# Kernel optimization log

Measured on AMD Instinct MI355X. Metric: run time of the kernel, lower is better.

The kernel has to match this reference:

```python
import jax, jax.numpy as jnp
import numpy as np
from jax.scipy.special import erfc

# ---- model constants (mirroring NeuroNN.__init__ defaults) ----
NEURON_NUM = 6000
RATIO = 0.8
NE = int(NEURON_NUM * RATIO)   # excitatory count (pref ordering: E first)
NI = NEURON_NUM - NE           # inhibitory count (connection blocks: first NI rows/cols)
SCALING_G = 1.0
W_FF = 30.0
SIG_EXT = 5.0
TAU = 1.0
TAU_REF = 1.0
T_INV = 1.0
VT, VR = 20.0, 10.0            # LIF threshold / reset (mV) used inside Ricciardi Phi
DT = 0.1
NMAX = 80                      # Euler2fixedpt total steps (fixed for jit)
NAVG = 30                      # convergence-averaging window
XTOL = 1e-5
XMIN = 1.0

# 64-pt Gauss-Legendre quadrature for the Ricciardi integral
_qn, _qw = np.polynomial.legendre.leggauss(64)
QN = jnp.asarray(_qn, jnp.float32)
QW = jnp.asarray(_qw, jnp.float32)
SQRT_PI = float(np.sqrt(np.pi))


def erfcx(y):
    """Scaled complementary error function exp(y^2)*erfc(y), fp32-safe."""
    y = jnp.clip(y, -9.0, 25.0)  # exp(81) still finite in fp32
    a = jnp.abs(y)
    a_s = jnp.minimum(a, 5.0)
    small = jnp.exp(a_s * a_s) * erfc(a_s)
    a_l = jnp.maximum(a, 5.0)
    large = (1.0 / (SQRT_PI * a_l)) * (1.0 - 0.5 / (a_l * a_l))
    f = jnp.where(a <= 5.0, small, large)
    return jnp.where(y >= 0.0, f, 2.0 * jnp.exp(y * y) - f)


def circ_gauss(x_deg, w):
    # circular gaussian with period 180 deg, same form as the z-row kernel
    return jnp.exp((jnp.cos(x_deg * jnp.pi / 90.0) - 1.0) / (4.0 * (jnp.pi / 180.0 * w) ** 2))


def phi(mu, sigma, tau, tau_ref):
    """Ricciardi LIF transfer: 1/(tau_ref + tau*sqrt(pi)*int_l^u erfcx(-x) dx)."""
    u = (VT - mu) / sigma
    l = (VR - mu) / sigma
    c = 0.5 * (u + l)
    h = 0.5 * (u - l)
    x = c[:, None] + h[:, None] * QN[None, :]          # [N, 64]
    integ = h * jnp.sum(QW[None, :] * erfcx(-x), axis=1)
    return 1.0 / (tau_ref + tau * SQRT_PI * jnp.maximum(integ, 0.0))


def setup_inputs() -> dict:
    key = jax.random.key(0)
    k1, k2, k3 = jax.random.split(key, 3)
    # hyperparameters = [J; P; w], exactly the module's init values
    hyperparameters = jnp.array([[1.99, 1.9, -1.01, -0.79],
                                 [0.11, 0.11, 0.45, 0.45],
                                 [32.0, 32.0, 32.0, 32.0]], dtype=jnp.float32)
    contrast = jax.random.uniform(k1, (1,), jnp.float32)                 # [0,1)
    grating_orientations = jax.random.uniform(k2, (1,), jnp.float32) * 180.0
    # self.pref: E then I linspace over [0,180)
    pref = np.concatenate([np.linspace(0.0, 180.0, NE, endpoint=False),
                           np.linspace(0.0, 180.0, NI, endpoint=False)]).astype(np.float32)
    preferred_orientations = jnp.asarray(pref)
    rand_u = jax.random.uniform(k3, (NEURON_NUM, NEURON_NUM), jnp.float32)
    return {"hyperparameters": hyperparameters, "contrast": contrast,
            "grating_orientations": grating_orientations,
            "preferred_orientations": preferred_orientations, "rand_u": rand_u}


def reference(hyperparameters, contrast, grating_orientations, preferred_orientations, rand_u):
    N = NEURON_NUM
    eff_p, prob_p, width_p = hyperparameters[0], hyperparameters[1], hyperparameters[2]
    i = jnp.arange(N)
    ri = (i < NI).astype(jnp.int32)                      # row block (1 if row < NI)
    conn = ri[:, None] + 2 * ri[None, :]                 # 0/1/2/3 block ids [N,N]
    # circulant roll: np.roll(z_row, i)[j] = z_row[(j-i) % N]
    idx = (i[None, :] - i[:, None]) % N                  # [N,N]
    conn_rolled = ri[:, None] + 2 * (idx < NI).astype(jnp.int32)
    thetas = jnp.linspace(0.0, jnp.pi - 0.01, N)
    cos_term = (jnp.cos(2.0 * thetas) - 1.0)[idx]        # gathered, rolled per row
    width_r = width_p[conn_rolled]
    Z = jnp.exp(cos_term / (4.0 * (jnp.pi / 180.0 * width_r) ** 2))
    # W[i,j] = J * sigmoid(32*(P * z_roll - U))
    W = eff_p[conn] * jax.nn.sigmoid(32.0 * (prob_p[conn] * Z - rand_u))
    W2 = W * W
    # stimulus -> feedforward input
    input_mean = contrast * 20.0 * SCALING_G * circ_gauss(
        grating_orientations - preferred_orientations, W_FF)          # [N]
    input_sd = SIG_EXT

    def step(r, _):
        mu = TAU * (W @ r) + input_mean
        sig = jnp.sqrt(TAU * (W2 @ r) + input_sd ** 2)
        dx = T_INV * (phi(mu, sig, TAU, TAU_REF) - r) * DT
        r2 = r + dx
        conv = jnp.max(jnp.abs(dx) / jnp.maximum(XMIN, jnp.abs(r2))) < XTOL
        return r2, conv

    r0 = jnp.zeros(N, jnp.float32)
    r_fp, convs = jax.lax.scan(step, r0, None, length=NMAX)
    avg_step = jnp.mean(convs[-NAVG:].astype(jnp.float32))
    return r_fp, avg_step
```

## Files before the change

### kernel.cpp

```cpp
#include <hip/hip_runtime.h>
#include <hip/hip_fp16.h>
#include <math.h>

#define NN    6000
#define NPAD  6144
#define NIB   1200
#define NMAXI 80
#define NAVGI 30
#define NBLK  250
#define NTHR  768

#define SQRT_PI_F 1.7724538509055160273f

typedef _Float16 half2_t __attribute__((ext_vector_type(2)));
typedef unsigned uvec8  __attribute__((ext_vector_type(8)));

__device__ __forceinline__ float erfcx_ref(float y) {
  y = fminf(fmaxf(y, -9.0f), 25.0f);
  float a   = fabsf(y);
  float a_s = fminf(a, 5.0f);
  float fsm = expf(a_s * a_s) * erfcf(a_s);
  float a_l = fmaxf(a, 5.0f);
  float flg = (1.0f / (SQRT_PI_F * a_l)) * (1.0f - 0.5f / (a_l * a_l));
  float f   = (a <= 5.0f) ? fsm : flg;
  return (y >= 0.0f) ? f : 2.0f * expf(y * y) - f;
}

__device__ __forceinline__ float dot2acc(unsigned w, unsigned r, float acc) {
#if defined(__has_builtin) && __has_builtin(__builtin_amdgcn_fdot2)
  return __builtin_amdgcn_fdot2(__builtin_bit_cast(half2_t, w),
                                __builtin_bit_cast(half2_t, r), acc, false);
#else
  half2_t wh = __builtin_bit_cast(half2_t, w);
  half2_t rh = __builtin_bit_cast(half2_t, r);
  return acc + (float)wh.x * (float)rh.x + (float)wh.y * (float)rh.y;
#endif
}

__device__ __forceinline__ unsigned pksq(unsigned w) {
  half2_t wh = __builtin_bit_cast(half2_t, w);
  half2_t s  = wh * wh;
  return __builtin_bit_cast(unsigned, s);
}

__device__ __forceinline__ void gbar(unsigned* cnt, unsigned* gen, int tid) {
  __syncthreads();
  if (tid == 0) {
    __builtin_amdgcn_fence(__ATOMIC_RELEASE, "agent");
    const unsigned g = __hip_atomic_load(gen, __ATOMIC_RELAXED,
                                         __HIP_MEMORY_SCOPE_AGENT);
    const unsigned old = __hip_atomic_fetch_add(cnt, 1u, __ATOMIC_RELAXED,
                                                __HIP_MEMORY_SCOPE_AGENT);
    if (old == NBLK - 1) {
      __hip_atomic_store(cnt, 0u, __ATOMIC_RELAXED, __HIP_MEMORY_SCOPE_AGENT);
      __hip_atomic_store(gen, g + 1u, __ATOMIC_RELEASE,
                         __HIP_MEMORY_SCOPE_AGENT);
    } else {
      while (__hip_atomic_load(gen, __ATOMIC_RELAXED,
                               __HIP_MEMORY_SCOPE_AGENT) == g)
        __builtin_amdgcn_s_sleep(2);
    }
    __builtin_amdgcn_fence(__ATOMIC_ACQUIRE, "agent");
  }
  __syncthreads();
}

__global__ __launch_bounds__(256) void init_kernel(
    const float* __restrict__ contrast, const float* __restrict__ grat,
    const float* __restrict__ pref, float* __restrict__ g0,
    float* __restrict__ g1, float* __restrict__ meanv,
    float* __restrict__ ctab, float* __restrict__ qn, float* __restrict__ qw,
    unsigned* __restrict__ conv, unsigned* __restrict__ bar)
{
  int t = blockIdx.x * 256 + threadIdx.x;
  if (t < NPAD) { g0[t] = 0.0f; g1[t] = 0.0f; }
  if (t < NN) {
    double th = (3.141592653589793 - 0.01) * (double)t / 5999.0;
    ctab[t] = cosf(2.0f * (float)th) - 1.0f;
    float d  = grat[0] - pref[t];
    float cg = (cosf(d * 3.14159265358979323846f / 90.0f) - 1.0f) / 1.0966227112321508f;
    meanv[t] = contrast[0] * 20.0f * expf(cg);
  }
  if (t < NMAXI) conv[t] = 0u;
  if (t < 2)     bar[t]  = 0u;
  if (blockIdx.x == 0 && threadIdx.x < 64) {
    int m = threadIdx.x;
    double x = cos(3.141592653589793 * (m + 0.75) / 64.5);
    double p0, p1, dp = 1.0;
    for (int it = 0; it < 60; ++it) {
      p0 = 1.0; p1 = x;
      for (int k = 2; k <= 64; ++k) {
        double p2 = ((2.0 * k - 1.0) * x * p1 - (k - 1.0) * p0) / (double)k;
        p0 = p1; p1 = p2;
      }
      dp = 64.0 * (x * p1 - p0) / (x * x - 1.0);
      double step = p1 / dp;
      x -= step;
      if (fabs(step) < 1e-15) break;
    }
    p0 = 1.0; p1 = x;
    for (int k = 2; k <= 64; ++k) {
      double p2 = ((2.0 * k - 1.0) * x * p1 - (k - 1.0) * p0) / (double)k;
      p0 = p1; p1 = p2;
    }
    dp = 64.0 * (x * p1 - p0) / (x * x - 1.0);
    double wgt = 2.0 / ((1.0 - x * x) * dp * dp);
    qn[63 - m] = (float)x;
    qw[63 - m] = (float)wgt;
  }
}

#define GENV(WV, ROW, V, EI, EE, PI, PE, DI, DE, UROW)                        \
  do {                                                                        \
    _Pragma("unroll")                                                         \
    for (int c_ = 0; c_ < 4; ++c_) {                                          \
      const int k_  = (V) * 4 + c_;                                           \
      const int j0_ = k_ * 256 + (lane << 2);                                 \
      float w_[4] = {0.0f, 0.0f, 0.0f, 0.0f};                                 \
      if (j0_ + 3 < NN) {                                                     \
        const float4 uv_ = *reinterpret_cast<const float4*>((UROW) + j0_);    \
        const float us_[4] = {uv_.x, uv_.y, uv_.z, uv_.w};                    \
        _Pragma("unroll")                                                     \
        for (int q_ = 0; q_ < 4; ++q_) {                                      \
          const int j_ = j0_ + q_;                                            \
          int idx_ = j_ - (ROW); idx_ += (idx_ < 0) ? NN : 0;                 \
          const float ct_   = ctabs[idx_];                                    \
          const float eff_  = (j_   < NIB) ? (EI) : (EE);                     \
          const float prob_ = (j_   < NIB) ? (PI) : (PE);                     \
          const float den_  = (idx_ < NIB) ? (DI) : (DE);                     \
          const float Z_  = expf(ct_ / den_);                                 \
          const float tt_ = 32.0f * (prob_ * Z_ - us_[q_]);                   \
          w_[q_] = eff_ / (1.0f + expf(-tt_));                                \
        }                                                                     \
      }                                                                       \
      half2_t h01_; h01_.x = (_Float16)w_[0]; h01_.y = (_Float16)w_[1];       \
      half2_t h23_; h23_.x = (_Float16)w_[2]; h23_.y = (_Float16)w_[3];       \
      WV[2 * c_]     = __builtin_bit_cast(unsigned, h01_);                    \
      WV[2 * c_ + 1] = __builtin_bit_cast(unsigned, h23_);                    \
    }                                                                         \
  } while (0)

#define ACC2(WAV, WBV, V)                                                     \
  do {                                                                        \
    _Pragma("unroll")                                                         \
    for (int c_ = 0; c_ < 4; ++c_) {                                          \
      const uint2 rr_ = rh2[((V) * 4 + c_) * 64 + lane];                      \
      muA  = dot2acc(WAV[2 * c_],       rr_.x, muA);                          \
      muA  = dot2acc(WAV[2 * c_ + 1],   rr_.y, muA);                          \
      varA = dot2acc(pksq(WAV[2 * c_]),     rr_.x, varA);                     \
      varA = dot2acc(pksq(WAV[2 * c_ + 1]), rr_.y, varA);                     \
      muB  = dot2acc(WBV[2 * c_],       rr_.x, muB);                          \
      muB  = dot2acc(WBV[2 * c_ + 1],   rr_.y, muB);                          \
      varB = dot2acc(pksq(WBV[2 * c_]),     rr_.x, varB);                     \
      varB = dot2acc(pksq(WBV[2 * c_ + 1]), rr_.y, varB);                     \
    }                                                                         \
  } while (0)

__global__ __launch_bounds__(NTHR, 3) void solve_kernel(
    const float* __restrict__ hyper, const float* __restrict__ randu,
    const float* __restrict__ ctab, const float* __restrict__ meanv,
    const float* __restrict__ qn, const float* __restrict__ qw,
    float* __restrict__ g0, float* __restrict__ g1,
    float* __restrict__ blkmax, unsigned* __restrict__ bar,
    float* __restrict__ out)
{
  const int tid  = threadIdx.x;
  const int lane = tid & 63;
  const int wv   = tid >> 6;
  const int rowA = blockIdx.x * 24 + wv * 2;
  const int rowB = rowA + 1;

  __shared__ float ctabs[NN];
  __shared__ uint2 rh2[NPAD / 4];
  __shared__ float wmax[12];
  __shared__ float sflag[NAVGI];

  {
    const float4* c4 = reinterpret_cast<const float4*>(ctab);
    float4* l4 = reinterpret_cast<float4*>(ctabs);
    for (int i = tid; i < NN / 4; i += NTHR) l4[i] = c4[i];
  }
  __syncthreads();

  const float qnl = qn[lane];
  const float qwl = qw[lane];
  const float meanA = meanv[rowA];
  const float meanB = meanv[rowB];

  uvec8 wa0, wa1, wa2, wa3, wa4, wa5, wb0, wb1, wb2, wb3, wb4, wb5;
  {
    const int   riA = (rowA < NIB) ? 1 : 0;
    const float eIa = hyper[2 + riA], eEa = hyper[0 + riA];
    const float pIa = hyper[6 + riA], pEa = hyper[4 + riA];
    const float cdg = 0.017453292519943295f;
    const float wIa = cdg * hyper[10 + riA], wEa = cdg * hyper[8 + riA];
    const float dIa = 4.0f * (wIa * wIa), dEa = 4.0f * (wEa * wEa);
    const float* urA = randu + (size_t)rowA * NN;
    GENV(wa0, rowA, 0, eIa, eEa, pIa, pEa, dIa, dEa, urA);
    GENV(wa1, rowA, 1, eIa, eEa, pIa, pEa, dIa, dEa, urA);
    GENV(wa2, rowA, 2, eIa, eEa, pIa, pEa, dIa, dEa, urA);
    GENV(wa3, rowA, 3, eIa, eEa, pIa, pEa, dIa, dEa, urA);
    GENV(wa4, rowA, 4, eIa, eEa, pIa, pEa, dIa, dEa, urA);
    GENV(wa5, rowA, 5, eIa, eEa, pIa, pEa, dIa, dEa, urA);
    const int   riB = (rowB < NIB) ? 1 : 0;
    const float eIb = hyper[2 + riB], eEb = hyper[0 + riB];
    const float pIb = hyper[6 + riB], pEb = hyper[4 + riB];
    const float wIb = cdg * hyper[10 + riB], wEb = cdg * hyper[8 + riB];
    const float dIb = 4.0f * (wIb * wIb), dEb = 4.0f * (wEb * wEb);
    const float* urB = randu + (size_t)rowB * NN;
    GENV(wb0, rowB, 0, eIb, eEb, pIb, pEb, dIb, dEb, urB);
    GENV(wb1, rowB, 1, eIb, eEb, pIb, pEb, dIb, dEb, urB);
    GENV(wb2, rowB, 2, eIb, eEb, pIb, pEb, dIb, dEb, urB);
    GENV(wb3, rowB, 3, eIb, eEb, pIb, pEb, dIb, dEb, urB);
    GENV(wb4, rowB, 4, eIb, eEb, pIb, pEb, dIb, dEb, urB);
    GENV(wb5, rowB, 5, eIb, eEb, pIb, pEb, dIb, dEb, urB);
  }

#pragma unroll 1
  for (int t = 0; t < NMAXI; ++t) {
    const float* rcur = (t & 1) ? g1 : g0;
    float*       rnxt = (t & 1) ? g0 : g1;

    {
      const float4* rc4 = reinterpret_cast<const float4*>(rcur);
      const float4 s0 = rc4[tid];
      const float4 s1 = rc4[tid + NTHR];
      half2_t a, b, c2, d2;
      a.x  = (_Float16)s0.x; a.y  = (_Float16)s0.y;
      b.x  = (_Float16)s0.z; b.y  = (_Float16)s0.w;
      c2.x = (_Float16)s1.x; c2.y = (_Float16)s1.y;
      d2.x = (_Float16)s1.z; d2.y = (_Float16)s1.w;
      uint2 p0, p1;
      p0.x = __builtin_bit_cast(unsigned, a);
      p0.y = __builtin_bit_cast(unsigned, b);
      p1.x = __builtin_bit_cast(unsigned, c2);
      p1.y = __builtin_bit_cast(unsigned, d2);
      rh2[tid]        = p0;
      rh2[tid + NTHR] = p1;
    }
    __syncthreads();

    float muA = 0.0f, varA = 0.0f, muB = 0.0f, varB = 0.0f;
    ACC2(wa0, wb0, 0);
    ACC2(wa1, wb1, 1);
    ACC2(wa2, wb2, 2);
    ACC2(wa3, wb3, 3);
    ACC2(wa4, wb4, 4);
    ACC2(wa5, wb5, 5);
#pragma unroll
    for (int off = 32; off > 0; off >>= 1) {
      muA  += __shfl_xor(muA, off);
      varA += __shfl_xor(varA, off);
      muB  += __shfl_xor(muB, off);
      varB += __shfl_xor(varB, off);
    }

    float ratioM = 0.0f;
#pragma unroll
    for (int rr = 0; rr < 2; ++rr) {
      const int   row  = rr ? rowB : rowA;
      float mu  = (rr ? muB : muA)  + (rr ? meanB : meanA);
      float var = (rr ? varB : varA) + 25.0f;
      const float sig = sqrtf(var);
      const float uu = (20.0f - mu) / sig;
      const float ll = (10.0f - mu) / sig;
      const float cc = 0.5f * (uu + ll);
      const float hh = 0.5f * (uu - ll);
      const float x = cc + hh * qnl;
      float term    = qwl * erfcx_ref(-x);
#pragma unroll
      for (int off = 32; off > 0; off >>= 1) term += __shfl_xor(term, off);
      const float integ = hh * term;
      const float phiv  = 1.0f / (1.0f + SQRT_PI_F * fmaxf(integ, 0.0f));

      const float rold = rcur[row];
      const float dx   = (phiv - rold) * 0.1f;
      const float rnew = rold + dx;
      ratioM = fmaxf(ratioM, fabsf(dx) / fmaxf(1.0f, fabsf(rnew)));
      if (lane == 0) {
        if (t == NMAXI - 1) out[row] = rnew;
        else                rnxt[row] = rnew;
      }
    }
    if (lane == 0) wmax[wv] = ratioM;
    __syncthreads();
    if (tid == 0) {
      float m = wmax[0];
#pragma unroll
      for (int q = 1; q < 12; ++q) m = fmaxf(m, wmax[q]);
      blkmax[(size_t)t * NBLK + blockIdx.x] = m;
    }
    gbar(bar, bar + 1, tid);
  }

  if (blockIdx.x == 0) {
#pragma unroll
    for (int s = 0; s < 3; ++s) {
      const int t = 50 + wv + 12 * s;
      if (t < NMAXI) {
        float m = 0.0f;
        for (int p = lane; p < NBLK; p += 64)
          m = fmaxf(m, blkmax[(size_t)t * NBLK + p]);
#pragma unroll
        for (int off = 32; off > 0; off >>= 1)
          m = fmaxf(m, __shfl_xor(m, off));
        if (lane == 0) sflag[t - 50] = (m < 1e-5f) ? 1.0f : 0.0f;
      }
    }
    __syncthreads();
    if (tid == 0) {
      float s = 0.0f;
#pragma unroll
      for (int q = 0; q < NAVGI; ++q) s += sflag[q];
      out[NN] = s / 30.0f;
    }
  }
}

__global__ __launch_bounds__(256) void genw_kernel(
    const float* __restrict__ hyper, const float* __restrict__ randu,
    const float* __restrict__ ctab, float* __restrict__ Wf)
{
  const int i  = blockIdx.x;
  const int ri = (i < NIB) ? 1 : 0;
  const float eA = hyper[0 + ri], eB = hyper[2 + ri];
  const float pA = hyper[4 + ri], pB = hyper[6 + ri];
  const float c  = 0.017453292519943295f;
  const float wA = c * hyper[8 + ri], wB = c * hyper[10 + ri];
  const float dA = 4.0f * (wA * wA), dB = 4.0f * (wB * wB);
  const float* urow = randu + (size_t)i * NN;
  for (int j4 = threadIdx.x * 4; j4 < NN; j4 += 1024) {
    float4 uv = *reinterpret_cast<const float4*>(urow + j4);
    float us[4] = {uv.x, uv.y, uv.z, uv.w};
    float res[4];
#pragma unroll
    for (int q = 0; q < 4; ++q) {
      int j   = j4 + q;
      int idx = j - i; idx += (idx < 0) ? NN : 0;
      float ct   = ctab[idx];
      float eff  = (j   < NIB) ? eB : eA;
      float prob = (j   < NIB) ? pB : pA;
      float den  = (idx < NIB) ? dB : dA;
      float Z  = expf(ct / den);
      float tt = 32.0f * (prob * Z - us[q]);
      res[q] = eff / (1.0f + expf(-tt));
    }
    *reinterpret_cast<float4*>(Wf + (size_t)i * NN + j4) =
        make_float4(res[0], res[1], res[2], res[3]);
  }
}

__global__ __launch_bounds__(256) void iter_kernel(
    const float* __restrict__ Wf, const float* __restrict__ rin,
    float* __restrict__ rout, const float* __restrict__ meanv,
    const float* __restrict__ qn, const float* __restrict__ qw,
    unsigned* __restrict__ convslot)
{
  const int row  = blockIdx.x;
  const int tid  = threadIdx.x;
  const int lane = tid & 63;
  const int wvid = tid >> 6;
  __shared__ float smu[4], svar[4];
  float mu = 0.0f, var = 0.0f;
  const float* wrow = Wf + (size_t)row * NN;
  float4 w[6], r4[6]; bool have[6];
#pragma unroll
  for (int k = 0; k < 6; ++k) {
    const int j = (tid << 2) + (k << 10);
    have[k] = (j < NN);
    if (have[k]) {
      w[k]  = *reinterpret_cast<const float4*>(wrow + j);
      r4[k] = *reinterpret_cast<const float4*>(rin + j);
    }
  }
#pragma unroll
  for (int k = 0; k < 6; ++k) if (have[k]) {
    mu  += w[k].x * r4[k].x + w[k].y * r4[k].y + w[k].z * r4[k].z + w[k].w * r4[k].w;
    var += w[k].x * w[k].x * r4[k].x + w[k].y * w[k].y * r4[k].y
         + w[k].z * w[k].z * r4[k].z + w[k].w * w[k].w * r4[k].w;
  }
#pragma unroll
  for (int off = 32; off > 0; off >>= 1) {
    mu  += __shfl_xor(mu, off);
    var += __shfl_xor(var, off);
  }
  if (lane == 0) { smu[wvid] = mu; svar[wvid] = var; }
  __syncthreads();
  if (tid < 64) {
    mu  = smu[0] + smu[1] + smu[2] + smu[3];
    var = svar[0] + svar[1] + svar[2] + svar[3];
    mu += meanv[row]; var += 25.0f;
    const float sig = sqrtf(var);
    const float uu = (20.0f - mu) / sig;
    const float ll = (10.0f - mu) / sig;
    const float cc = 0.5f * (uu + ll);
    const float hh = 0.5f * (uu - ll);
    const float x = cc + hh * qn[lane];
    float term    = qw[lane] * erfcx_ref(-x);
#pragma unroll
    for (int off = 32; off > 0; off >>= 1) term += __shfl_xor(term, off);
    const float integ = hh * term;
    const float phiv  = 1.0f / (1.0f + SQRT_PI_F * fmaxf(integ, 0.0f));
    const float rold = rin[row];
    const float dx   = (phiv - rold) * 0.1f;
    const float rnew = rold + dx;
    if (lane == 0) {
      rout[row] = rnew;
      const float ratio = fabsf(dx) / fmaxf(1.0f, fabsf(rnew));
      atomicMax(convslot, __float_as_uint(ratio));
    }
  }
}

__global__ __launch_bounds__(256) void final_kernel(
    const float* __restrict__ rfin, const unsigned* __restrict__ conv,
    float* __restrict__ out)
{
  int t = blockIdx.x * 256 + threadIdx.x;
  if (t < NN) out[t] = rfin[t];
  if (t == 6000) {
    float s = 0.0f;
    for (int k = NMAXI - NAVGI; k < NMAXI; ++k)
      s += (__uint_as_float(conv[k]) < 1e-5f) ? 1.0f : 0.0f;
    out[NN] = s / 30.0f;
  }
}

extern "C" void kernel_launch(void* const* d_in, const int* in_sizes, int n_in,
                              void* d_out, int out_size, void* d_ws, size_t ws_size,
                              hipStream_t stream) {
  const float* hyper    = (const float*)d_in[0];
  const float* contrast = (const float*)d_in[1];
  const float* grat     = (const float*)d_in[2];
  const float* pref     = (const float*)d_in[3];
  const float* randu    = (const float*)d_in[4];
  float* out = (float*)d_out;

  char* ws = (char*)d_ws;
  float*    g0     = (float*)(ws + 0);
  float*    g1     = (float*)(ws + 24576);
  float*    mn     = (float*)(ws + 49152);
  float*    ctab   = (float*)(ws + 73152);
  float*    qn     = (float*)(ws + 97152);
  float*    qw     = (float*)(ws + 97408);
  unsigned* conv   = (unsigned*)(ws + 97664);
  unsigned* bar    = (unsigned*)(ws + 97984);
  float*    blkmax = (float*)(ws + 98304);
  float*    Wf     = (float*)(ws + 262144);

  init_kernel<<<24, 256, 0, stream>>>(contrast, grat, pref, g0, g1, mn, ctab,
                                      qn, qw, conv, bar);

  {
    const float* a_hyper = hyper;  const float* a_randu = randu;
    const float* a_ctab  = ctab;   const float* a_mn    = mn;
    const float* a_qn    = qn;     const float* a_qw    = qw;
    float* a_g0 = g0; float* a_g1 = g1; float* a_bm = blkmax;
    unsigned* a_bar = bar; float* a_out = out;
    void* args[11] = {&a_hyper, &a_randu, &a_ctab, &a_mn, &a_qn, &a_qw,
                      &a_g0, &a_g1, &a_bm, &a_bar, &a_out};
    hipError_t err = hipLaunchCooperativeKernel(
        (const void*)solve_kernel, dim3(NBLK), dim3(NTHR), args, 0, stream);
    if (err == hipSuccess) return;
  }

  genw_kernel<<<NN, 256, 0, stream>>>(hyper, randu, ctab, Wf);
  float* rb[2] = {g0, g1};
  for (int t = 0; t < NMAXI; ++t) {
    const float* rin = rb[t & 1];
    float*       rou = rb[(t + 1) & 1];
    iter_kernel<<<NN, 256, 0, stream>>>(Wf, rin, rou, mn, qn, qw, conv + t);
  }
  final_kernel<<<24, 256, 0, stream>>>(rb[0], conv, out);
}
```

Measured before the change: 1.652 ms.

## Process three rows per wave with 512-thread blocks instead of two

```diff
diff --git a/kernel.cpp b/kernel.cpp
--- a/kernel.cpp
+++ b/kernel.cpp
@@ -8,7 +8,7 @@
 #define NMAXI 80
 #define NAVGI 30
 #define NBLK  250
-#define NTHR  768
+#define NTHR  512
 
 #define SQRT_PI_F 1.7724538509055160273f
 
@@ -140,7 +140,7 @@
     }                                                                         \
   } while (0)
 
-#define ACC2(WAV, WBV, V)                                                     \
+#define ACC3(WAV, WBV, WCV, V)                                                \
   do {                                                                        \
     _Pragma("unroll")                                                         \
     for (int c_ = 0; c_ < 4; ++c_) {                                          \
@@ -153,10 +153,14 @@
       muB  = dot2acc(WBV[2 * c_ + 1],   rr_.y, muB);                          \
       varB = dot2acc(pksq(WBV[2 * c_]),     rr_.x, varB);                     \
       varB = dot2acc(pksq(WBV[2 * c_ + 1]), rr_.y, varB);                     \
+      muC  = dot2acc(WCV[2 * c_],       rr_.x, muC);                          \
+      muC  = dot2acc(WCV[2 * c_ + 1],   rr_.y, muC);                          \
+      varC = dot2acc(pksq(WCV[2 * c_]),     rr_.x, varC);                     \
+      varC = dot2acc(pksq(WCV[2 * c_ + 1]), rr_.y, varC);                     \
     }                                                                         \
   } while (0)
 
-__global__ __launch_bounds__(NTHR, 3) void solve_kernel(
+__global__ __launch_bounds__(NTHR, 2) void solve_kernel(
     const float* __restrict__ hyper, const float* __restrict__ randu,
     const float* __restrict__ ctab, const float* __restrict__ meanv,
     const float* __restrict__ qn, const float* __restrict__ qw,
@@ -167,12 +171,13 @@
   const int tid  = threadIdx.x;
   const int lane = tid & 63;
   const int wv   = tid >> 6;
-  const int rowA = blockIdx.x * 24 + wv * 2;
+  const int rowA = blockIdx.x * 24 + wv * 3;
   const int rowB = rowA + 1;
+  const int rowC = rowA + 2;
 
   __shared__ float ctabs[NN];
   __shared__ uint2 rh2[NPAD / 4];
-  __shared__ float wmax[12];
+  __shared__ float wmax[8];
   __shared__ float sflag[NAVGI];
 
   {
@@ -186,34 +191,55 @@
   const float qwl = qw[lane];
   const float meanA = meanv[rowA];
   const float meanB = meanv[rowB];
-
-  uvec8 wa0, wa1, wa2, wa3, wa4, wa5, wb0, wb1, wb2, wb3, wb4, wb5;
+  const float meanC = meanv[rowC];
+
+  uvec8 wa0, wa1, wa2, wa3, wa4, wa5;
+  uvec8 wb0, wb1, wb2, wb3, wb4, wb5;
+  uvec8 wc0, wc1, wc2, wc3, wc4, wc5;
   {
-    const int   riA = (rowA < NIB) ? 1 : 0;
-    const float eIa = hyper[2 + riA], eEa = hyper[0 + riA];
-    const float pIa = hyper[6 + riA], pEa = hyper[4 + riA];
     const float cdg = 0.017453292519943295f;
-    const float wIa = cdg * hyper[10 + riA], wEa = cdg * hyper[8 + riA];
-    const float dIa = 4.0f * (wIa * wIa), dEa = 4.0f * (wEa * wEa);
-    const float* urA = randu + (size_t)rowA * NN;
-    GENV(wa0, rowA, 0, eIa, eEa, pIa, pEa, dIa, dEa, urA);
-    GENV(wa1, rowA, 1, eIa, eEa, pIa, pEa, dIa, dEa, urA);
-    GENV(wa2, rowA, 2, eIa, eEa, pIa, pEa, dIa, dEa, urA);
-    GENV(wa3, rowA, 3, eIa, eEa, pIa, pEa, dIa, dEa, urA);
-    GENV(wa4, rowA, 4, eIa, eEa, pIa, pEa, dIa, dEa, urA);
-    GENV(wa5, rowA, 5, eIa, eEa, pIa, pEa, dIa, dEa, urA);
-    const int   riB = (rowB < NIB) ? 1 : 0;
-    const float eIb = hyper[2 + riB], eEb = hyper[0 + riB];
-    const float pIb = hyper[6 + riB], pEb = hyper[4 + riB];
-    const float wIb = cdg * hyper[10 + riB], wEb = cdg * hyper[8 + riB];
-    const float dIb = 4.0f * (wIb * wIb), dEb = 4.0f * (wEb * wEb);
-    const float* urB = randu + (size_t)rowB * NN;
-    GENV(wb0, rowB, 0, eIb, eEb, pIb, pEb, dIb, dEb, urB);
-    GENV(wb1, rowB, 1, eIb, eEb, pIb, pEb, dIb, dEb, urB);
-    GENV(wb2, rowB, 2, eIb, eEb, pIb, pEb, dIb, dEb, urB);
-    GENV(wb3, rowB, 3, eIb, eEb, pIb, pEb, dIb, dEb, urB);
-    GENV(wb4, rowB, 4, eIb, eEb, pIb, pEb, dIb, dEb, urB);
-    GENV(wb5, rowB, 5, eIb, eEb, pIb, pEb, dIb, dEb, urB);
+    {
+      const int   ri = (rowA < NIB) ? 1 : 0;
+      const float eI = hyper[2 + ri], eE = hyper[0 + ri];
+      const float pI = hyper[6 + ri], pE = hyper[4 + ri];
+      const float wI = cdg * hyper[10 + ri], wE = cdg * hyper[8 + ri];
+      const float dI = 4.0f * (wI * wI), dE = 4.0f * (wE * wE);
+      const float* ur = randu + (size_t)rowA * NN;
+      GENV(wa0, rowA, 0, eI, eE, pI, pE, dI, dE, ur);
+      GENV(wa1, rowA, 1, eI, eE, pI, pE, dI, dE, ur);
+      GENV(wa2, rowA, 2, eI, eE, pI, pE, dI, dE, ur);
+      GENV(wa3, rowA, 3, eI, eE, pI, pE, dI, dE, ur);
+      GENV(wa4, rowA, 4, eI, eE, pI, pE, dI, dE, ur);
+      GENV(wa5, rowA, 5, eI, eE, pI, pE, dI, dE, ur);
+    }
+    {
+      const int   ri = (rowB < NIB) ? 1 : 0;
+      const float eI = hyper[2 + ri], eE = hyper[0 + ri];
+      const float pI = hyper[6 + ri], pE = hyper[4 + ri];
+      const float wI = cdg * hyper[10 + ri], wE = cdg * hyper[8 + ri];
+      const float dI = 4.0f * (wI * wI), dE = 4.0f * (wE * wE);
+      const float* ur = randu + (size_t)rowB * NN;
+      GENV(wb0, rowB, 0, eI, eE, pI, pE, dI, dE, ur);
+      GENV(wb1, rowB, 1, eI, eE, pI, pE, dI, dE, ur);
+      GENV(wb2, rowB, 2, eI, eE, pI, pE, dI, dE, ur);
+      GENV(wb3, rowB, 3, eI, eE, pI, pE, dI, dE, ur);
+      GENV(wb4, rowB, 4, eI, eE, pI, pE, dI, dE, ur);
+      GENV(wb5, rowB, 5, eI, eE, pI, pE, dI, dE, ur);
+    }
+    {
+      const int   ri = (rowC < NIB) ? 1 : 0;
+      const float eI = hyper[2 + ri], eE = hyper[0 + ri];
+      const float pI = hyper[6 + ri], pE = hyper[4 + ri];
+      const float wI = cdg * hyper[10 + ri], wE = cdg * hyper[8 + ri];
+      const float dI = 4.0f * (wI * wI), dE = 4.0f * (wE * wE);
+      const float* ur = randu + (size_t)rowC * NN;
+      GENV(wc0, rowC, 0, eI, eE, pI, pE, dI, dE, ur);
+      GENV(wc1, rowC, 1, eI, eE, pI, pE, dI, dE, ur);
+      GENV(wc2, rowC, 2, eI, eE, pI, pE, dI, dE, ur);
+      GENV(wc3, rowC, 3, eI, eE, pI, pE, dI, dE, ur);
+      GENV(wc4, rowC, 4, eI, eE, pI, pE, dI, dE, ur);
+      GENV(wc5, rowC, 5, eI, eE, pI, pE, dI, dE, ur);
+    }
   }
 
 #pragma unroll 1
@@ -223,44 +249,45 @@
 
     {
       const float4* rc4 = reinterpret_cast<const float4*>(rcur);
-      const float4 s0 = rc4[tid];
-      const float4 s1 = rc4[tid + NTHR];
-      half2_t a, b, c2, d2;
-      a.x  = (_Float16)s0.x; a.y  = (_Float16)s0.y;
-      b.x  = (_Float16)s0.z; b.y  = (_Float16)s0.w;
-      c2.x = (_Float16)s1.x; c2.y = (_Float16)s1.y;
-      d2.x = (_Float16)s1.z; d2.y = (_Float16)s1.w;
-      uint2 p0, p1;
-      p0.x = __builtin_bit_cast(unsigned, a);
-      p0.y = __builtin_bit_cast(unsigned, b);
-      p1.x = __builtin_bit_cast(unsigned, c2);
-      p1.y = __builtin_bit_cast(unsigned, d2);
-      rh2[tid]        = p0;
-      rh2[tid + NTHR] = p1;
+#pragma unroll
+      for (int s = 0; s < 3; ++s) {
+        const float4 s0 = rc4[tid + s * NTHR];
+        half2_t a, b;
+        a.x = (_Float16)s0.x; a.y = (_Float16)s0.y;
+        b.x = (_Float16)s0.z; b.y = (_Float16)s0.w;
+        uint2 p;
+        p.x = __builtin_bit_cast(unsigned, a);
+        p.y = __builtin_bit_cast(unsigned, b);
+        rh2[tid + s * NTHR] = p;
+      }
     }
     __syncthreads();
 
     float muA = 0.0f, varA = 0.0f, muB = 0.0f, varB = 0.0f;
-    ACC2(wa0, wb0, 0);
-    ACC2(wa1, wb1, 1);
-    ACC2(wa2, wb2, 2);
-    ACC2(wa3, wb3, 3);
-    ACC2(wa4, wb4, 4);
-    ACC2(wa5, wb5, 5);
+    float muC = 0.0f, varC = 0.0f;
+    ACC3(wa0, wb0, wc0, 0);
+    ACC3(wa1, wb1, wc1, 1);
+    ACC3(wa2, wb2, wc2, 2);
+    ACC3(wa3, wb3, wc3, 3);
+    ACC3(wa4, wb4, wc4, 4);
+    ACC3(wa5, wb5, wc5, 5);
 #pragma unroll
     for (int off = 32; off > 0; off >>= 1) {
       muA  += __shfl_xor(muA, off);
       varA += __shfl_xor(varA, off);
       muB  += __shfl_xor(muB, off);
       varB += __shfl_xor(varB, off);
+      muC  += __shfl_xor(muC, off);
+      varC += __shfl_xor(varC, off);
     }
 
     float ratioM = 0.0f;
 #pragma unroll
-    for (int rr = 0; rr < 2; ++rr) {
-      const int   row  = rr ? rowB : rowA;
-      float mu  = (rr ? muB : muA)  + (rr ? meanB : meanA);
-      float var = (rr ? varB : varA) + 25.0f;
+    for (int rr = 0; rr < 3; ++rr) {
+      const int   row = (rr == 0) ? rowA : (rr == 1) ? rowB : rowC;
+      float mu  = ((rr == 0) ? muA  : (rr == 1) ? muB  : muC)
+                + ((rr == 0) ? meanA : (rr == 1) ? meanB : meanC);
+      float var = ((rr == 0) ? varA : (rr == 1) ? varB : varC) + 25.0f;
       const float sig = sqrtf(var);
       const float uu = (20.0f - mu) / sig;
       const float ll = (10.0f - mu) / sig;
@@ -287,7 +314,7 @@
     if (tid == 0) {
       float m = wmax[0];
 #pragma unroll
-      for (int q = 1; q < 12; ++q) m = fmaxf(m, wmax[q]);
+      for (int q = 1; q < 8; ++q) m = fmaxf(m, wmax[q]);
       blkmax[(size_t)t * NBLK + blockIdx.x] = m;
     }
     gbar(bar, bar + 1, tid);
@@ -295,8 +322,8 @@
 
   if (blockIdx.x == 0) {
 #pragma unroll
-    for (int s = 0; s < 3; ++s) {
-      const int t = 50 + wv + 12 * s;
+    for (int s = 0; s < 4; ++s) {
+      const int t = 50 + wv + 8 * s;
       if (t < NMAXI) {
         float m = 0.0f;
         for (int p = lane; p < NBLK; p += 64)
```

After: 1.723 ms. 1.04x slower.
